# Kernel optimization log

Measured on AMD Instinct MI355X. Metric: run time of the kernel, lower is better.

## Reference

```python
import jax, jax.numpy as jnp
import numpy as np

B, D, H, MEM = 8192, 512, 8, 16
HD = D // H
LN_EPS = 1e-6  # flax.linen.LayerNorm default


def layer_norm(x, scale, bias):
    mu = jnp.mean(x, axis=-1, keepdims=True)
    var = jnp.mean(jnp.square(x - mu), axis=-1, keepdims=True)
    return (x - mu) * jax.lax.rsqrt(var + LN_EPS) * scale + bias


def setup_inputs() -> dict:
    key = jax.random.key(0)
    ks = jax.random.split(key, 12)
    s = 0.02
    return {
        "mem": jax.random.normal(ks[0], (B, MEM, D), jnp.float32),
        "ssum": jax.random.normal(ks[1], (B, D), jnp.float32),
        "x": jax.random.normal(ks[2], (B, D), jnp.float32),
        "alpha": jnp.zeros((D,), jnp.float32),   # flax param init zeros
        "lam": jnp.zeros((D,), jnp.float32),     # flax param init zeros
        "ln1_scale": jnp.ones((D,), jnp.float32),
        "ln1_bias": jnp.zeros((D,), jnp.float32),
        "ln2_scale": jnp.ones((D,), jnp.float32),
        "ln2_bias": jnp.zeros((D,), jnp.float32),
        "wq": jax.random.normal(ks[3], (D, D), jnp.float32) * s,
        "bq": jnp.zeros((D,), jnp.float32),
        "wk": jax.random.normal(ks[4], (D, D), jnp.float32) * s,
        "bk": jnp.zeros((D,), jnp.float32),
        "wv": jax.random.normal(ks[5], (D, D), jnp.float32) * s,
        "bv": jnp.zeros((D,), jnp.float32),
        "wo": jax.random.normal(ks[6], (D, D), jnp.float32) * s,
        "bo": jnp.zeros((D,), jnp.float32),
        "w1": jax.random.normal(ks[7], (D, 4 * D), jnp.float32) * s,
        "b1": jnp.zeros((4 * D,), jnp.float32),
        "w2": jax.random.normal(ks[8], (4 * D, D), jnp.float32) * s,
        "b2": jnp.zeros((D,), jnp.float32),
    }


def reference(mem, ssum, x, alpha, lam, ln1_scale, ln1_bias, ln2_scale, ln2_bias,
              wq, bq, wk, bk, wv, bv, wo, bo, w1, b1, w2, b2):
    # gated input
    x_in = x + ssum * jax.nn.sigmoid(alpha)                       # [B, D]
    # sliding-window memory update
    updated_mem = jnp.concatenate([mem[:, 1:, :], x_in[:, None, :]], axis=1)  # [B, MEM, D]
    # pre-attn LayerNorm
    y = layer_norm(x_in, ln1_scale, ln1_bias)                      # [B, D]
    # multi-head attention: query len 1, kv = updated_mem (len MEM)
    q = (y @ wq + bq).reshape(B, 1, H, HD)
    k = (updated_mem @ wk + bk).reshape(B, MEM, H, HD)
    v = (updated_mem @ wv + bv).reshape(B, MEM, H, HD)
    scores = jnp.einsum('bqhd,bkhd->bhqk', q, k) / jnp.sqrt(jnp.float32(HD))
    attn = jax.nn.softmax(scores, axis=-1)                         # [B, H, 1, MEM]
    ctx = jnp.einsum('bhqk,bkhd->bqhd', attn, v).reshape(B, 1, D)
    y = (ctx @ wo + bo)[:, 0, :]                                   # [B, D]
    x_mid = x_in + y
    # MLP block
    y = layer_norm(x_mid, ln2_scale, ln2_bias)
    y = jax.nn.gelu(y @ w1 + b1)  # flax nn.gelu default: approximate
    y = y @ w2 + b2
    x_out = x_mid + y
    # gated state update
    lam_s = jax.nn.sigmoid(lam)
    new_ssum = ssum * lam_s + x_out * (1.0 - lam_s)
    return (updated_mem, new_ssum, x_out)
```

## Files before the change

kernel.cpp:

```cpp
#include <hip/hip_runtime.h>

typedef unsigned short u16;
typedef __attribute__((ext_vector_type(8))) short bf16x8;
typedef __attribute__((ext_vector_type(4))) float floatx4;
typedef __attribute__((ext_vector_type(4))) unsigned u32x4;

#define DEV __device__ __forceinline__

constexpr int BDIM = 8192;
constexpr int D    = 512;
constexpr int H    = 8;
constexpr int HDIM = 64;
constexpr int MEMN = 16;
constexpr int DFF  = 2048;

DEV u16 f2b(float f){
  union { float f; unsigned u; } v; v.f = f;
  unsigned u = v.u;
  return (u16)((u + 0x7fffu + ((u >> 16) & 1u)) >> 16);
}
DEV float b2f(u16 s){
  union { unsigned u; float f; } v; v.u = ((unsigned)s) << 16;
  return v.f;
}
DEV float b2f_lo(unsigned u){ union { unsigned x; float f; } v; v.x = u << 16; return v.f; }
DEV float b2f_hi(unsigned u){ union { unsigned x; float f; } v; v.x = u & 0xffff0000u; return v.f; }
DEV float sigmoidf_(float x){ return 1.f / (1.f + expf(-x)); }

__global__ __launch_bounds__(256) void transpose_f32_bf16(
    const float* __restrict__ src, u16* __restrict__ dst, int R, int C)
{
  __shared__ float tl[32][33];
  int tx = threadIdx.x & 31, ty = threadIdx.x >> 5;
  int c0 = blockIdx.x * 32, r0 = blockIdx.y * 32;
  #pragma unroll
  for (int i = 0; i < 32; i += 8)
    tl[ty + i][tx] = src[(size_t)(r0 + ty + i) * C + c0 + tx];
  __syncthreads();
  #pragma unroll
  for (int i = 0; i < 32; i += 8)
    dst[(size_t)(c0 + ty + i) * R + r0 + tx] = f2b(tl[tx][ty + i]);
}

__global__ __launch_bounds__(256) void convert_f32_bf16(
    const float* __restrict__ src, u16* __restrict__ dst, int n)
{
  for (int i = blockIdx.x * 256 + threadIdx.x; i < n; i += gridDim.x * 256)
    dst[i] = f2b(src[i]);
}

__global__ __launch_bounds__(256) void k_xin_ln1(
    const float* __restrict__ x, const float* __restrict__ ssum,
    const float* __restrict__ alpha, const float* __restrict__ g,
    const float* __restrict__ bta,
    float* __restrict__ x_in, u16* __restrict__ y1)
{
  int row = blockIdx.x * 4 + (threadIdx.x >> 6);
  int lane = threadIdx.x & 63;
  size_t base = (size_t)row * D;
  float v[8];
  float s1 = 0.f, s2 = 0.f;
  #pragma unroll
  for (int hh = 0; hh < 2; ++hh){
    int c = hh * 256 + lane * 4;
    float4 xv = *(const float4*)(x + base + c);
    float4 sv = *(const float4*)(ssum + base + c);
    float4 av = *(const float4*)(alpha + c);
    float t0 = xv.x + sv.x * sigmoidf_(av.x);
    float t1 = xv.y + sv.y * sigmoidf_(av.y);
    float t2 = xv.z + sv.z * sigmoidf_(av.z);
    float t3 = xv.w + sv.w * sigmoidf_(av.w);
    v[hh*4+0] = t0; v[hh*4+1] = t1; v[hh*4+2] = t2; v[hh*4+3] = t3;
    s1 += t0 + t1 + t2 + t3;
    s2 += t0*t0 + t1*t1 + t2*t2 + t3*t3;
  }
  #pragma unroll
  for (int m = 1; m < 64; m <<= 1){
    s1 += __shfl_xor(s1, m);
    s2 += __shfl_xor(s2, m);
  }
  float mu = s1 * (1.f / D);
  float var = s2 * (1.f / D) - mu * mu;
  float rs = rsqrtf(var + 1e-6f);
  #pragma unroll
  for (int hh = 0; hh < 2; ++hh){
    int c = hh * 256 + lane * 4;
    float4 gv = *(const float4*)(g + c);
    float4 bv = *(const float4*)(bta + c);
    float4 xi = { v[hh*4+0], v[hh*4+1], v[hh*4+2], v[hh*4+3] };
    *(float4*)(x_in + base + c) = xi;
    ushort4 o;
    o.x = f2b((xi.x - mu) * rs * gv.x + bv.x);
    o.y = f2b((xi.y - mu) * rs * gv.y + bv.y);
    o.z = f2b((xi.z - mu) * rs * gv.z + bv.z);
    o.w = f2b((xi.w - mu) * rs * gv.w + bv.w);
    *(ushort4*)(y1 + base + c) = o;
  }
}

__global__ __launch_bounds__(256) void k_ln(
    const float* __restrict__ in, const float* __restrict__ g,
    const float* __restrict__ bta, u16* __restrict__ out)
{
  int row = blockIdx.x * 4 + (threadIdx.x >> 6);
  int lane = threadIdx.x & 63;
  size_t base = (size_t)row * D;
  float v[8];
  float s1 = 0.f, s2 = 0.f;
  #pragma unroll
  for (int hh = 0; hh < 2; ++hh){
    int c = hh * 256 + lane * 4;
    float4 xv = *(const float4*)(in + base + c);
    v[hh*4+0] = xv.x; v[hh*4+1] = xv.y; v[hh*4+2] = xv.z; v[hh*4+3] = xv.w;
    s1 += xv.x + xv.y + xv.z + xv.w;
    s2 += xv.x*xv.x + xv.y*xv.y + xv.z*xv.z + xv.w*xv.w;
  }
  #pragma unroll
  for (int m = 1; m < 64; m <<= 1){
    s1 += __shfl_xor(s1, m);
    s2 += __shfl_xor(s2, m);
  }
  float mu = s1 * (1.f / D);
  float var = s2 * (1.f / D) - mu * mu;
  float rs = rsqrtf(var + 1e-6f);
  #pragma unroll
  for (int hh = 0; hh < 2; ++hh){
    int c = hh * 256 + lane * 4;
    float4 gv = *(const float4*)(g + c);
    float4 bv = *(const float4*)(bta + c);
    ushort4 o;
    o.x = f2b((v[hh*4+0] - mu) * rs * gv.x + bv.x);
    o.y = f2b((v[hh*4+1] - mu) * rs * gv.y + bv.y);
    o.z = f2b((v[hh*4+2] - mu) * rs * gv.z + bv.z);
    o.w = f2b((v[hh*4+3] - mu) * rs * gv.w + bv.w);
    *(ushort4*)(out + base + c) = o;
  }
}

__global__ __launch_bounds__(256, 4) void k_attn(
    const float* __restrict__ mem, const float* __restrict__ x_in,
    const u16* __restrict__ T, float* __restrict__ umem, u16* __restrict__ wsum)
{
  __shared__ __attribute__((aligned(16))) float mem_l[MEMN][516];
  __shared__ __attribute__((aligned(16))) float attn_l[H][16];

  int b = blockIdx.x;
  int t = threadIdx.x;

  const float* msrc = mem + (size_t)b * MEMN * D;
  float* mdst = umem + (size_t)b * MEMN * D;
  #pragma unroll
  for (int j = 0; j < 8; ++j){
    int i = t + j * 256;
    int r = i >> 7, c = (i & 127) * 4;
    floatx4 val;
    if (r < MEMN - 1)
      val = __builtin_nontemporal_load((const floatx4*)(msrc + (size_t)(r + 1) * D + c));
    else
      val = *(const floatx4*)(x_in + (size_t)b * D + c);
    __builtin_nontemporal_store(val, (floatx4*)(mdst + (size_t)r * D + c));
    *(floatx4*)&mem_l[r][c] = val;
  }
  __syncthreads();

  {
    int lane = t & 63, w = t >> 6;
    int k = lane & 15;
    int dh = (lane >> 4) & 1;
    int h = 2 * w + (lane >> 5);
    const u16* Tg = T + (size_t)b * (H * D) + h * D + dh * 256;
    const float* mrow = &mem_l[k][dh * 256];
    float acc = 0.f;
    #pragma unroll 4
    for (int s = 0; s < 32; ++s){
      floatx4 m0 = *(const floatx4*)(mrow + s * 8);
      floatx4 m1 = *(const floatx4*)(mrow + s * 8 + 4);
      u32x4 tv = *(const u32x4*)(Tg + s * 8);
      acc += m0.x * b2f_lo(tv.x); acc += m0.y * b2f_hi(tv.x);
      acc += m0.z * b2f_lo(tv.y); acc += m0.w * b2f_hi(tv.y);
      acc += m1.x * b2f_lo(tv.z); acc += m1.y * b2f_hi(tv.z);
      acc += m1.z * b2f_lo(tv.w); acc += m1.w * b2f_hi(tv.w);
    }
    acc += __shfl_xor(acc, 16);
    float sc = acc * 0.125f;
    float mx = sc;
    #pragma unroll
    for (int m = 1; m < 16; m <<= 1) mx = fmaxf(mx, __shfl_xor(mx, m));
    float e = expf(sc - mx);
    float sm = e;
    #pragma unroll
    for (int m = 1; m < 16; m <<= 1) sm += __shfl_xor(sm, m);
    if (dh == 0) attn_l[h][k] = e / sm;
  }
  __syncthreads();

  {
    int d0 = (t & 127) * 4;
    int hp = t >> 7;
    float acc4[4][4] = {};
    #pragma unroll
    for (int kq = 0; kq < 4; ++kq){
      floatx4 av[4];
      #pragma unroll
      for (int hh = 0; hh < 4; ++hh)
        av[hh] = *(const floatx4*)&attn_l[hp + hh * 2][kq * 4];
      #pragma unroll
      for (int kk = 0; kk < 4; ++kk){
        floatx4 mv = *(const floatx4*)&mem_l[kq * 4 + kk][d0];
        #pragma unroll
        for (int hh = 0; hh < 4; ++hh){
          float a = (kk == 0) ? av[hh].x : (kk == 1) ? av[hh].y
                  : (kk == 2) ? av[hh].z : av[hh].w;
          acc4[hh][0] += a * mv.x;
          acc4[hh][1] += a * mv.y;
          acc4[hh][2] += a * mv.z;
          acc4[hh][3] += a * mv.w;
        }
      }
    }
    u16* wb = wsum + (size_t)b * (H * D);
    #pragma unroll
    for (int hh = 0; hh < 4; ++hh){
      int h = hp + hh * 2;
      ushort4 o;
      o.x = f2b(acc4[hh][0]); o.y = f2b(acc4[hh][1]);
      o.z = f2b(acc4[hh][2]); o.w = f2b(acc4[hh][3]);
      *(ushort4*)(wb + h * D + d0) = o;
    }
  }
}

struct EpiQ {
  const float* bq; u16* out;
  DEV void apply(int z, int r, int c, float v) const {
    out[(size_t)r * D + c] = f2b(v + bq[c]);
  }
};
struct EpiT {
  u16* out;
  DEV void apply(int z, int r, int c, float v) const {
    out[(size_t)r * (H * D) + z * D + c] = f2b(v);
  }
};
struct EpiCtx {
  const float* bv; u16* out;
  DEV void apply(int z, int r, int c, float v) const {
    out[(size_t)r * D + z * HDIM + c] = f2b(v + bv[z * HDIM + c]);
  }
};
struct EpiOut {
  const float* bo; const float* x_in; float* x_mid;
  DEV void apply(int z, int r, int c, float v) const {
    size_t i = (size_t)r * D + c;
    x_mid[i] = x_in[i] + v + bo[c];
  }
};
struct EpiMlp1 {
  const float* b1; u16* out;
  DEV void apply(int z, int r, int c, float v) const {
    float u = v + b1[c];
    float t = tanhf(0.79788456080286536f * (u + 0.044715f * u * u * u));
    out[(size_t)r * DFF + c] = f2b(0.5f * u * (1.f + t));
  }
};
struct EpiMlp2 {
  const float* b2; const float* x_mid; const float* ssum; const float* lam;
  float* x_out; float* nss;
  DEV void apply(int z, int r, int c, float v) const {
    size_t i = (size_t)r * D + c;
    float xo = x_mid[i] + v + b2[c];
    x_out[i] = xo;
    float ls = 1.f / (1.f + expf(-lam[c]));
    nss[i] = ssum[i] * ls + xo * (1.f - ls);
  }
};

template<int BM, int BN, int WMW, int WNW, typename Epi>
__global__ __launch_bounds__(256) void gemm_bt(
    const u16* __restrict__ A, const u16* __restrict__ BT,
    int K, int lda, int ldb, int a_zoff, int b_zoff, Epi epi)
{
  constexpr int MI = BM / (WMW * 16);
  constexpr int NI = BN / (WNW * 16);
  constexpr int LDT = 40;
  __shared__ u16 As[BM * LDT];
  __shared__ u16 Bs[BN * LDT];

  const int z = blockIdx.z;
  A  += (size_t)z * a_zoff;
  BT += (size_t)z * b_zoff;
  const int bm0 = blockIdx.y * BM;
  const int bn0 = blockIdx.x * BN;
  const int tid = threadIdx.x;
  const int lane = tid & 63;
  const int wvid = tid >> 6;
  const int wm = wvid % WMW, wn = wvid / WMW;
  const int ln = lane & 15, quad = lane >> 4;

  floatx4 acc[MI][NI] = {};

  constexpr int ASLOT = BM * 4;
  constexpr int TSLOT = ASLOT + BN * 4;

  for (int kt = 0; kt < K; kt += 32){
    if (kt) __syncthreads();
    for (int s = tid; s < TSLOT; s += 256){
      bool isB = s >= ASLOT;
      int s2 = isB ? s - ASLOT : s;
      int row = s2 >> 2, seg = s2 & 3;
      const u16* src = isB ? BT + (size_t)(bn0 + row) * ldb + kt + seg * 8
                           : A  + (size_t)(bm0 + row) * lda + kt + seg * 8;
      u16* dst = (isB ? Bs : As) + row * LDT + seg * 8;
      *(uint4*)dst = *(const uint4*)src;
    }
    __syncthreads();
    bf16x8 af[MI], bfm[NI];
    #pragma unroll
    for (int mi = 0; mi < MI; ++mi)
      af[mi] = *(const bf16x8*)&As[(wm * MI * 16 + mi * 16 + ln) * LDT + quad * 8];
    #pragma unroll
    for (int ni = 0; ni < NI; ++ni)
      bfm[ni] = *(const bf16x8*)&Bs[(wn * NI * 16 + ni * 16 + ln) * LDT + quad * 8];
    #pragma unroll
    for (int mi = 0; mi < MI; ++mi)
      #pragma unroll
      for (int ni = 0; ni < NI; ++ni)
        acc[mi][ni] = __builtin_amdgcn_mfma_f32_16x16x32_bf16(af[mi], bfm[ni], acc[mi][ni], 0, 0, 0);
  }

  #pragma unroll
  for (int mi = 0; mi < MI; ++mi){
    int row = bm0 + wm * MI * 16 + mi * 16 + quad * 4;
    #pragma unroll
    for (int ni = 0; ni < NI; ++ni){
      int col = bn0 + wn * NI * 16 + ni * 16 + ln;
      #pragma unroll
      for (int r = 0; r < 4; ++r)
        epi.apply(z, row + r, col, acc[mi][ni][r]);
    }
  }
}

extern "C" void kernel_launch(void* const* d_in, const int* in_sizes, int n_in,
                              void* d_out, int out_size, void* d_ws, size_t ws_size,
                              hipStream_t stream)
{
  (void)in_sizes; (void)n_in; (void)out_size; (void)ws_size;
  const float* mem   = (const float*)d_in[0];
  const float* ssum  = (const float*)d_in[1];
  const float* x     = (const float*)d_in[2];
  const float* alpha = (const float*)d_in[3];
  const float* lam   = (const float*)d_in[4];
  const float* g1    = (const float*)d_in[5];
  const float* bl1   = (const float*)d_in[6];
  const float* g2    = (const float*)d_in[7];
  const float* bl2   = (const float*)d_in[8];
  const float* wq    = (const float*)d_in[9];
  const float* bq    = (const float*)d_in[10];
  const float* wk    = (const float*)d_in[11];
  const float* wv    = (const float*)d_in[13];
  const float* bv    = (const float*)d_in[14];
  const float* wo    = (const float*)d_in[15];
  const float* bo    = (const float*)d_in[16];
  const float* w1    = (const float*)d_in[17];
  const float* b1    = (const float*)d_in[18];
  const float* w2    = (const float*)d_in[19];
  const float* b2    = (const float*)d_in[20];

  float* out_umem = (float*)d_out;
  float* out_nss  = out_umem + (size_t)BDIM * MEMN * D;
  float* out_x    = out_nss + (size_t)BDIM * D;

  constexpr size_t MiB = 1024ull * 1024ull;
  char* ws = (char*)d_ws;
  u16*   wqT  = (u16*)(ws + 0);
  u16*   wkC  = (u16*)(ws + 512 * 1024);
  u16*   wvT  = (u16*)(ws + 1 * MiB);
  u16*   woT  = (u16*)(ws + 1536 * 1024);
  u16*   w1T  = (u16*)(ws + 2 * MiB);
  u16*   w2T  = (u16*)(ws + 4 * MiB);
  float* x_in = (float*)(ws + 6 * MiB);
  float* x_mid= (float*)(ws + 22 * MiB);
  u16*   y1   = (u16*)(ws + 38 * MiB);
  u16*   Qb   = (u16*)(ws + 46 * MiB);
  u16*   ctx  = (u16*)(ws + 54 * MiB);
  u16*   Tb   = (u16*)(ws + 62 * MiB);
  u16*   wsum = (u16*)(ws + 126 * MiB);
  u16*   y2   = Qb;
  u16*   Hmid = Tb;

  transpose_f32_bf16<<<dim3(16, 16), 256, 0, stream>>>(wq, wqT, 512, 512);
  transpose_f32_bf16<<<dim3(16, 16), 256, 0, stream>>>(wv, wvT, 512, 512);
  transpose_f32_bf16<<<dim3(16, 16), 256, 0, stream>>>(wo, woT, 512, 512);
  transpose_f32_bf16<<<dim3(64, 16), 256, 0, stream>>>(w1, w1T, 512, 2048);
  transpose_f32_bf16<<<dim3(16, 64), 256, 0, stream>>>(w2, w2T, 2048, 512);
  convert_f32_bf16<<<256, 256, 0, stream>>>(wk, wkC, D * D);

  k_xin_ln1<<<BDIM / 4, 256, 0, stream>>>(x, ssum, alpha, g1, bl1, x_in, y1);

  gemm_bt<64, 64, 2, 2, EpiQ><<<dim3(8, 128, 1), 256, 0, stream>>>(
      y1, wqT, 512, 512, 512, 0, 0, EpiQ{bq, Qb});

  gemm_bt<128, 128, 2, 2, EpiT><<<dim3(4, 64, 8), 256, 0, stream>>>(
      Qb, wkC, 64, 512, 512, 64, 64, EpiT{Tb});

  k_attn<<<BDIM, 256, 0, stream>>>(mem, x_in, Tb, out_umem, wsum);

  gemm_bt<64, 64, 2, 2, EpiCtx><<<dim3(1, 128, 8), 256, 0, stream>>>(
      wsum, wvT, 512, H * D, 512, 512, 64 * 512, EpiCtx{bv, ctx});

  gemm_bt<64, 64, 2, 2, EpiOut><<<dim3(8, 128, 1), 256, 0, stream>>>(
      ctx, woT, 512, 512, 512, 0, 0, EpiOut{bo, x_in, x_mid});

  k_ln<<<BDIM / 4, 256, 0, stream>>>(x_mid, g2, bl2, y2);

  gemm_bt<128, 128, 2, 2, EpiMlp1><<<dim3(16, 64, 1), 256, 0, stream>>>(
      y2, w1T, 512, 512, 512, 0, 0, EpiMlp1{b1, Hmid});

  gemm_bt<64, 64, 2, 2, EpiMlp2><<<dim3(8, 128, 1), 256, 0, stream>>>(
      Hmid, w2T, 2048, 2048, 2048, 0, 0,
      EpiMlp2{b2, x_mid, ssum, lam, out_x, out_nss});
}
```

Measured before the change: 817.1 us.

## Merge weight prep with LN1 into one launch; shrink and swizzle attn LDS

Folds the five weight transposes, the wk conversion and the x_in/LN1 kernel into a single launch that dispatches on block index, removing six kernel launches. In the attention kernel, only the 15 shifted memory rows go into LDS, using an XOR-swizzled layout without padding. The 16th row (x_in) is read directly from global memory. The smaller LDS footprint lets the launch bound rise to 5 blocks per SM, at the cost of extra branching and global reads of x_in.

```diff
diff --git a/kernel.cpp b/kernel.cpp
--- a/kernel.cpp
+++ b/kernel.cpp
@@ -27,36 +27,48 @@
 DEV float b2f_hi(unsigned u){ union { unsigned x; float f; } v; v.x = u & 0xffff0000u; return v.f; }
 DEV float sigmoidf_(float x){ return 1.f / (1.f + expf(-x)); }
 
-__global__ __launch_bounds__(256) void transpose_f32_bf16(
-    const float* __restrict__ src, u16* __restrict__ dst, int R, int C)
-{
-  __shared__ float tl[32][33];
-  int tx = threadIdx.x & 31, ty = threadIdx.x >> 5;
-  int c0 = blockIdx.x * 32, r0 = blockIdx.y * 32;
-  #pragma unroll
-  for (int i = 0; i < 32; i += 8)
-    tl[ty + i][tx] = src[(size_t)(r0 + ty + i) * C + c0 + tx];
-  __syncthreads();
-  #pragma unroll
-  for (int i = 0; i < 32; i += 8)
-    dst[(size_t)(c0 + ty + i) * R + r0 + tx] = f2b(tl[tx][ty + i]);
-}
-
-__global__ __launch_bounds__(256) void convert_f32_bf16(
-    const float* __restrict__ src, u16* __restrict__ dst, int n)
-{
-  for (int i = blockIdx.x * 256 + threadIdx.x; i < n; i += gridDim.x * 256)
-    dst[i] = f2b(src[i]);
-}
-
-__global__ __launch_bounds__(256) void k_xin_ln1(
+__global__ __launch_bounds__(256) void k_prep(
+    const float* __restrict__ wq, const float* __restrict__ wv,
+    const float* __restrict__ wo, const float* __restrict__ w1,
+    const float* __restrict__ w2, const float* __restrict__ wk,
+    u16* __restrict__ wqT, u16* __restrict__ wvT, u16* __restrict__ woT,
+    u16* __restrict__ w1T, u16* __restrict__ w2T, u16* __restrict__ wkC,
     const float* __restrict__ x, const float* __restrict__ ssum,
     const float* __restrict__ alpha, const float* __restrict__ g,
     const float* __restrict__ bta,
     float* __restrict__ x_in, u16* __restrict__ y1)
 {
-  int row = blockIdx.x * 4 + (threadIdx.x >> 6);
-  int lane = threadIdx.x & 63;
+  __shared__ float tl[32][33];
+  int blk = blockIdx.x;
+  int t = threadIdx.x;
+
+  if (blk < 2816 || (blk >= 2816 && blk < 3072)){
+    if (blk < 2816){
+      const float* src; u16* dst; int C, bx, by;
+      if (blk < 256)      { src = wq; dst = wqT; C = 512;  bx = blk & 15;          by = blk >> 4; }
+      else if (blk < 512) { src = wv; dst = wvT; C = 512;  bx = (blk-256) & 15;    by = (blk-256) >> 4; }
+      else if (blk < 768) { src = wo; dst = woT; C = 512;  bx = (blk-512) & 15;    by = (blk-512) >> 4; }
+      else if (blk < 1792){ src = w1; dst = w1T; C = 2048; bx = (blk-768) & 63;    by = (blk-768) >> 6; }
+      else                { src = w2; dst = w2T; C = 512;  bx = (blk-1792) & 15;   by = (blk-1792) >> 4; }
+      int R = (blk >= 1792 && blk < 2816) ? 2048 : 512;
+      int tx = t & 31, ty = t >> 5;
+      int c0 = bx * 32, r0 = by * 32;
+      #pragma unroll
+      for (int i = 0; i < 32; i += 8)
+        tl[ty + i][tx] = src[(size_t)(r0 + ty + i) * C + c0 + tx];
+      __syncthreads();
+      #pragma unroll
+      for (int i = 0; i < 32; i += 8)
+        dst[(size_t)(c0 + ty + i) * R + r0 + tx] = f2b(tl[tx][ty + i]);
+    } else {
+      for (int i = (blk - 2816) * 256 + t; i < D * D; i += 256 * 256)
+        wkC[i] = f2b(wk[i]);
+    }
+    return;
+  }
+
+  int row = (blk - 3072) * 4 + (t >> 6);
+  int lane = t & 63;
   size_t base = (size_t)row * D;
   float v[8];
   float s1 = 0.f, s2 = 0.f;
@@ -137,11 +149,11 @@
   }
 }
 
-__global__ __launch_bounds__(256, 4) void k_attn(
+__global__ __launch_bounds__(256, 5) void k_attn(
     const float* __restrict__ mem, const float* __restrict__ x_in,
     const u16* __restrict__ T, float* __restrict__ umem, u16* __restrict__ wsum)
 {
-  __shared__ __attribute__((aligned(16))) float mem_l[MEMN][516];
+  __shared__ __attribute__((aligned(16))) float mem_l[15 * 512];
   __shared__ __attribute__((aligned(16))) float attn_l[H][16];
 
   int b = blockIdx.x;
@@ -149,17 +161,20 @@
 
   const float* msrc = mem + (size_t)b * MEMN * D;
   float* mdst = umem + (size_t)b * MEMN * D;
+  const float* xb = x_in + (size_t)b * D;
+
   #pragma unroll
   for (int j = 0; j < 8; ++j){
     int i = t + j * 256;
     int r = i >> 7, c = (i & 127) * 4;
     floatx4 val;
-    if (r < MEMN - 1)
+    if (r < 15)
       val = __builtin_nontemporal_load((const floatx4*)(msrc + (size_t)(r + 1) * D + c));
     else
-      val = *(const floatx4*)(x_in + (size_t)b * D + c);
+      val = *(const floatx4*)(xb + c);
     __builtin_nontemporal_store(val, (floatx4*)(mdst + (size_t)r * D + c));
-    *(floatx4*)&mem_l[r][c] = val;
+    if (r < 15)
+      *(floatx4*)&mem_l[r * 512 + (((c >> 2) ^ (r & 7)) << 2)] = val;
   }
   __syncthreads();
 
@@ -169,17 +184,33 @@
     int dh = (lane >> 4) & 1;
     int h = 2 * w + (lane >> 5);
     const u16* Tg = T + (size_t)b * (H * D) + h * D + dh * 256;
-    const float* mrow = &mem_l[k][dh * 256];
     float acc = 0.f;
-    #pragma unroll 4
-    for (int s = 0; s < 32; ++s){
-      floatx4 m0 = *(const floatx4*)(mrow + s * 8);
-      floatx4 m1 = *(const floatx4*)(mrow + s * 8 + 4);
-      u32x4 tv = *(const u32x4*)(Tg + s * 8);
-      acc += m0.x * b2f_lo(tv.x); acc += m0.y * b2f_hi(tv.x);
-      acc += m0.z * b2f_lo(tv.y); acc += m0.w * b2f_hi(tv.y);
-      acc += m1.x * b2f_lo(tv.z); acc += m1.y * b2f_hi(tv.z);
-      acc += m1.z * b2f_lo(tv.w); acc += m1.w * b2f_hi(tv.w);
+    if (k < 15){
+      const float* mrow = &mem_l[k * 512];
+      int xr = k & 7;
+      #pragma unroll 4
+      for (int s = 0; s < 32; ++s){
+        int fi = dh * 64 + s * 2;
+        floatx4 m0 = *(const floatx4*)(mrow + ((fi ^ xr) << 2));
+        floatx4 m1 = *(const floatx4*)(mrow + (((fi + 1) ^ xr) << 2));
+        u32x4 tv = *(const u32x4*)(Tg + s * 8);
+        acc += m0.x * b2f_lo(tv.x); acc += m0.y * b2f_hi(tv.x);
+        acc += m0.z * b2f_lo(tv.y); acc += m0.w * b2f_hi(tv.y);
+        acc += m1.x * b2f_lo(tv.z); acc += m1.y * b2f_hi(tv.z);
+        acc += m1.z * b2f_lo(tv.w); acc += m1.w * b2f_hi(tv.w);
+      }
+    } else {
+      const float* mrow = xb + dh * 256;
+      #pragma unroll 4
+      for (int s = 0; s < 32; ++s){
+        floatx4 m0 = *(const floatx4*)(mrow + s * 8);
+        floatx4 m1 = *(const floatx4*)(mrow + s * 8 + 4);
+        u32x4 tv = *(const u32x4*)(Tg + s * 8);
+        acc += m0.x * b2f_lo(tv.x); acc += m0.y * b2f_hi(tv.x);
+        acc += m0.z * b2f_lo(tv.y); acc += m0.w * b2f_hi(tv.y);
+        acc += m1.x * b2f_lo(tv.z); acc += m1.y * b2f_hi(tv.z);
+        acc += m1.z * b2f_lo(tv.w); acc += m1.w * b2f_hi(tv.w);
+      }
     }
     acc += __shfl_xor(acc, 16);
     float sc = acc * 0.125f;
@@ -197,6 +228,7 @@
   {
     int d0 = (t & 127) * 4;
     int hp = t >> 7;
+    int fi = d0 >> 2;
     float acc4[4][4] = {};
     #pragma unroll
     for (int kq = 0; kq < 4; ++kq){
@@ -204,9 +236,12 @@
       #pragma unroll
       for (int hh = 0; hh < 4; ++hh)
         av[hh] = *(const floatx4*)&attn_l[hp + hh * 2][kq * 4];
+      const int kmax = (kq == 3) ? 3 : 4;
       #pragma unroll
       for (int kk = 0; kk < 4; ++kk){
-        floatx4 mv = *(const floatx4*)&mem_l[kq * 4 + kk][d0];
+        if (kk >= kmax) break;
+        int row = kq * 4 + kk;
+        floatx4 mv = *(const floatx4*)&mem_l[row * 512 + ((fi ^ (row & 7)) << 2)];
         #pragma unroll
         for (int hh = 0; hh < 4; ++hh){
           float a = (kk == 0) ? av[hh].x : (kk == 1) ? av[hh].y
@@ -216,6 +251,17 @@
           acc4[hh][2] += a * mv.z;
           acc4[hh][3] += a * mv.w;
         }
+      }
+    }
+    {
+      floatx4 xv = *(const floatx4*)(xb + d0);
+      #pragma unroll
+      for (int hh = 0; hh < 4; ++hh){
+        float a = attn_l[hp + hh * 2][15];
+        acc4[hh][0] += a * xv.x;
+        acc4[hh][1] += a * xv.y;
+        acc4[hh][2] += a * xv.z;
+        acc4[hh][3] += a * xv.w;
       }
     }
     u16* wb = wsum + (size_t)b * (H * D);
@@ -389,14 +435,9 @@
   u16*   y2   = Qb;
   u16*   Hmid = Tb;
 
-  transpose_f32_bf16<<<dim3(16, 16), 256, 0, stream>>>(wq, wqT, 512, 512);
-  transpose_f32_bf16<<<dim3(16, 16), 256, 0, stream>>>(wv, wvT, 512, 512);
-  transpose_f32_bf16<<<dim3(16, 16), 256, 0, stream>>>(wo, woT, 512, 512);
-  transpose_f32_bf16<<<dim3(64, 16), 256, 0, stream>>>(w1, w1T, 512, 2048);
-  transpose_f32_bf16<<<dim3(16, 64), 256, 0, stream>>>(w2, w2T, 2048, 512);
-  convert_f32_bf16<<<256, 256, 0, stream>>>(wk, wkC, D * D);
-
-  k_xin_ln1<<<BDIM / 4, 256, 0, stream>>>(x, ssum, alpha, g1, bl1, x_in, y1);
+  k_prep<<<3072 + BDIM / 4, 256, 0, stream>>>(
+      wq, wv, wo, w1, w2, wk, wqT, wvT, woT, w1T, w2T, wkC,
+      x, ssum, alpha, g1, bl1, x_in, y1);
 
   gemm_bt<64, 64, 2, 2, EpiQ><<<dim3(8, 128, 1), 256, 0, stream>>>(
       y1, wqT, 512, 512, 512, 0, 0, EpiQ{bq, Qb});
```

New measurement: 902.8 us. 1.1x slower.
